# Performance work log

Hardware: AMD Instinct MI355X
Metric: run time of the kernel (lower is better)

## Reference

```python
import jax, jax.numpy as jnp
import numpy as np

N_NODES = 50000
N_EDGES = 800000
NFEAT, NHID, NCLASS = 512, 256, 128
N_UV = 2048


def gcn_layer(x, adj_row, adj_col, adj_val, W, b):
    # support = x @ W ; out = A @ support (sparse COO spmm) + b
    support = x @ W                                   # [N, out]
    msgs = adj_val[:, None] * support[adj_col]        # [E, out]
    out = jax.ops.segment_sum(msgs, adj_row, num_segments=N_NODES)
    return out + b


def setup_inputs() -> dict:
    key = jax.random.key(0)
    ks = jax.random.split(key, 12)
    u = jax.random.randint(ks[0], (N_UV,), 0, N_NODES)
    v = jax.random.randint(ks[1], (N_UV,), 0, N_NODES)
    x = jax.random.normal(ks[2], (N_NODES, NFEAT), dtype=jnp.float32)
    adj_row = jnp.sort(jax.random.randint(ks[3], (N_EDGES,), 0, N_NODES))
    adj_col = jax.random.randint(ks[4], (N_EDGES,), 0, N_NODES)
    adj_val = jax.random.uniform(ks[5], (N_EDGES,), dtype=jnp.float32)
    s1 = 1.0 / np.sqrt(NHID)
    s2 = 1.0 / np.sqrt(NCLASS)
    W1 = jax.random.uniform(ks[6], (NFEAT, NHID), minval=-s1, maxval=s1, dtype=jnp.float32)
    b1 = jax.random.uniform(ks[7], (NHID,), minval=-s1, maxval=s1, dtype=jnp.float32)
    W2 = jax.random.uniform(ks[8], (NHID, NCLASS), minval=-s2, maxval=s2, dtype=jnp.float32)
    b2 = jax.random.uniform(ks[9], (NCLASS,), minval=-s2, maxval=s2, dtype=jnp.float32)
    We = jax.random.normal(ks[10], (NCLASS, NCLASS), dtype=jnp.float32) * (1.0 / np.sqrt(NCLASS))
    return {"u": u, "v": v, "x": x, "adj_row": adj_row, "adj_col": adj_col,
            "adj_val": adj_val, "W1": W1, "b1": b1, "W2": W2, "b2": b2, "We": We}


def reference(u, v, x, adj_row, adj_col, adj_val, W1, b1, W2, b2, We):
    # layer 1: GCN + ReLU (dropout is identity in eval mode)
    h = jax.nn.relu(gcn_layer(x, adj_row, adj_col, adj_val, W1, b1))
    # layer 2: GCN
    z = gcn_layer(h, adj_row, adj_col, adj_val, W2, b2)          # [N, nclass]
    # edge scoring: sigmoid(w_edge(z[u]) @ z[v].T)
    zu = z[u] @ We.T                                             # [U, nclass] (nn.Linear: x @ W.T)
    zv = z[v]                                                    # [V, nclass]
    p_uv = jax.nn.sigmoid(zu @ zv.T)                             # [U, V]
    return p_uv
```

## Files before the change

### kernel.cpp

```cpp
#include <hip/hip_runtime.h>
#include <hip/hip_bf16.h>
#include <math.h>

#define N_NODES 50000
#define N_EDGES 800000
#define NFEAT   512
#define NHID    256
#define NCLASS  128
#define N_UV    2048

#define Q24_SCALE  524288.0f
#define Q24_INV    1.9073486328125e-6f

typedef __bf16    bf16x8 __attribute__((ext_vector_type(8)));
typedef short     s16x8  __attribute__((ext_vector_type(8)));
typedef float     f32x4  __attribute__((ext_vector_type(4)));

__device__ __forceinline__ unsigned short bf16_rn(float f) {
  unsigned u = __float_as_uint(f);
  u += 0x7fffu + ((u >> 16) & 1u);
  return (unsigned short)(u >> 16);
}
__device__ __forceinline__ float bf16_to_f(unsigned short h) {
  return __uint_as_float(((unsigned)h) << 16);
}

#define LDSPAD 40

template <bool ASPLIT, bool BSPLIT, int OMODE>
__global__ __launch_bounds__(256, 2) void gemm_mfma_split(
    const float* __restrict__ Af,
    const unsigned short* __restrict__ Ahi, const unsigned short* __restrict__ Alo,
    const float* __restrict__ BTf,
    const unsigned short* __restrict__ BThi, const unsigned short* __restrict__ BTlo,
    float* __restrict__ C, unsigned char* __restrict__ Cq, int M, int N, int K) {
  __shared__ unsigned short sAh[128 * LDSPAD];
  __shared__ unsigned short sAl[128 * LDSPAD];
  __shared__ unsigned short sBh[128 * LDSPAD];
  __shared__ unsigned short sBl[128 * LDSPAD];

  const int tid  = threadIdx.x;
  const int lane = tid & 63;
  const int wave = tid >> 6;
  const int wm   = (wave >> 1) << 6;
  const int wn   = (wave & 1) << 6;
  const int lm   = lane & 15;
  const int quad = lane >> 4;
  const int m0   = blockIdx.y * 128;
  const int n0   = blockIdx.x * 128;

  const int r32 = tid >> 3;
  const int c32 = (tid & 7) * 4;
  const int r16 = tid >> 2;
  const int c16 = (tid & 3) * 8;

  float4 pA[4]; s16x8 pAh[2], pAl[2];
  float4 pB[4]; s16x8 pBh[2], pBl[2];

  f32x4 acc[4][4];
#pragma unroll
  for (int i = 0; i < 4; ++i)
#pragma unroll
    for (int j = 0; j < 4; ++j)
#pragma unroll
      for (int r = 0; r < 4; ++r) acc[i][j][r] = 0.f;

#define LOAD_TILE(k0)                                                          \
  do {                                                                         \
    if (ASPLIT) {                                                              \
      _Pragma("unroll") for (int p = 0; p < 4; ++p) {                          \
        const int m = m0 + p * 32 + r32;                                       \
        pA[p] = make_float4(0.f, 0.f, 0.f, 0.f);                               \
        if (m < M) pA[p] = *(const float4*)&Af[(size_t)m * K + (k0) + c32];    \
      }                                                                        \
    } else {                                                                   \
      _Pragma("unroll") for (int p = 0; p < 2; ++p) {                          \
        const int m = m0 + p * 64 + r16;                                       \
        _Pragma("unroll") for (int e = 0; e < 8; ++e) { pAh[p][e] = 0; pAl[p][e] = 0; } \
        if (m < M) {                                                           \
          pAh[p] = *(const s16x8*)&Ahi[(size_t)m * K + (k0) + c16];            \
          pAl[p] = *(const s16x8*)&Alo[(size_t)m * K + (k0) + c16];            \
        }                                                                      \
      }                                                                        \
    }                                                                          \
    if (BSPLIT) {                                                              \
      _Pragma("unroll") for (int p = 0; p < 4; ++p) {                          \
        const int n = n0 + p * 32 + r32;                                       \
        pB[p] = *(const float4*)&BTf[(size_t)n * K + (k0) + c32];              \
      }                                                                        \
    } else {                                                                   \
      _Pragma("unroll") for (int p = 0; p < 2; ++p) {                          \
        pBh[p] = *(const s16x8*)&BThi[(size_t)(n0 + p * 64 + r16) * K + (k0) + c16]; \
        pBl[p] = *(const s16x8*)&BTlo[(size_t)(n0 + p * 64 + r16) * K + (k0) + c16]; \
      }                                                                        \
    }                                                                          \
  } while (0)

#define SPLIT4(v, hv, lv)                                                      \
  hv.x = bf16_rn(v.x); lv.x = bf16_rn(v.x - bf16_to_f(hv.x));                  \
  hv.y = bf16_rn(v.y); lv.y = bf16_rn(v.y - bf16_to_f(hv.y));                  \
  hv.z = bf16_rn(v.z); lv.z = bf16_rn(v.z - bf16_to_f(hv.z));                  \
  hv.w = bf16_rn(v.w); lv.w = bf16_rn(v.w - bf16_to_f(hv.w));

#define STORE_TILE()                                                           \
  do {                                                                         \
    if (ASPLIT) {                                                              \
      _Pragma("unroll") for (int p = 0; p < 4; ++p) {                          \
        ushort4 hv, lv; SPLIT4(pA[p], hv, lv);                                 \
        const int row = p * 32 + r32;                                          \
        *(ushort4*)&sAh[row * LDSPAD + c32] = hv;                              \
        *(ushort4*)&sAl[row * LDSPAD + c32] = lv;                              \
      }                                                                        \
    } else {                                                                   \
      _Pragma("unroll") for (int p = 0; p < 2; ++p) {                          \
        const int row = p * 64 + r16;                                          \
        *(s16x8*)&sAh[row * LDSPAD + c16] = pAh[p];                            \
        *(s16x8*)&sAl[row * LDSPAD + c16] = pAl[p];                            \
      }                                                                        \
    }                                                                          \
    if (BSPLIT) {                                                              \
      _Pragma("unroll") for (int p = 0; p < 4; ++p) {                          \
        ushort4 hv, lv; SPLIT4(pB[p], hv, lv);                                 \
        const int row = p * 32 + r32;                                          \
        *(ushort4*)&sBh[row * LDSPAD + c32] = hv;                              \
        *(ushort4*)&sBl[row * LDSPAD + c32] = lv;                              \
      }                                                                        \
    } else {                                                                   \
      _Pragma("unroll") for (int p = 0; p < 2; ++p) {                          \
        const int row = p * 64 + r16;                                          \
        *(s16x8*)&sBh[row * LDSPAD + c16] = pBh[p];                            \
        *(s16x8*)&sBl[row * LDSPAD + c16] = pBl[p];                            \
      }                                                                        \
    }                                                                          \
  } while (0)

  LOAD_TILE(0);

  for (int k0 = 0; k0 < K; k0 += 32) {
    if (k0) __syncthreads();
    STORE_TILE();
    __syncthreads();
    if (k0 + 32 < K) LOAD_TILE(k0 + 32);

    bf16x8 aH[4], aL[4], bH[4], bL[4];
#pragma unroll
    for (int i = 0; i < 4; ++i) {
      const int r = wm + i * 16 + lm;
      aH[i] = __builtin_bit_cast(bf16x8, *(const s16x8*)&sAh[r * LDSPAD + quad * 8]);
      aL[i] = __builtin_bit_cast(bf16x8, *(const s16x8*)&sAl[r * LDSPAD + quad * 8]);
    }
#pragma unroll
    for (int j = 0; j < 4; ++j) {
      const int r = wn + j * 16 + lm;
      bH[j] = __builtin_bit_cast(bf16x8, *(const s16x8*)&sBh[r * LDSPAD + quad * 8]);
      bL[j] = __builtin_bit_cast(bf16x8, *(const s16x8*)&sBl[r * LDSPAD + quad * 8]);
    }
#pragma unroll
    for (int i = 0; i < 4; ++i)
#pragma unroll
      for (int j = 0; j < 4; ++j) {
        acc[i][j] = __builtin_amdgcn_mfma_f32_16x16x32_bf16(aH[i], bH[j], acc[i][j], 0, 0, 0);
        acc[i][j] = __builtin_amdgcn_mfma_f32_16x16x32_bf16(aH[i], bL[j], acc[i][j], 0, 0, 0);
        acc[i][j] = __builtin_amdgcn_mfma_f32_16x16x32_bf16(aL[i], bH[j], acc[i][j], 0, 0, 0);
      }
  }

  const size_t qstride = (size_t)M * N;
#pragma unroll
  for (int i = 0; i < 4; ++i)
#pragma unroll
    for (int j = 0; j < 4; ++j) {
      const int col = n0 + wn + j * 16 + lm;
#pragma unroll
      for (int r = 0; r < 4; ++r) {
        const int row = m0 + wm + i * 16 + quad * 4 + r;
        if (row < M) {
          float v = acc[i][j][r];
          if (OMODE == 1) {
            v = 1.f / (1.f + expf(-v));
            C[(size_t)row * N + col] = v;
          } else if (OMODE == 2) {
            int q = __float2int_rn(v * Q24_SCALE);
            q = q > 8388607 ? 8388607 : (q < -8388608 ? -8388608 : q);
            const size_t o = (size_t)row * N + col;
            Cq[o]               = (unsigned char)(q & 0xFF);
            Cq[qstride + o]     = (unsigned char)((q >> 8) & 0xFF);
            Cq[2 * qstride + o] = (unsigned char)((q >> 16) & 0xFF);
          } else {
            C[(size_t)row * N + col] = v;
          }
        }
      }
    }
#undef LOAD_TILE
#undef STORE_TILE
#undef SPLIT4
}

__global__ __launch_bounds__(256) void prep_all(
    const int* __restrict__ rows, int* __restrict__ row_ptr,
    const float* __restrict__ W1, unsigned short* __restrict__ W1Thi,
    unsigned short* __restrict__ W1Tlo,
    const float* __restrict__ W2, unsigned short* __restrict__ W2Thi,
    unsigned short* __restrict__ W2Tlo) {
  const int idx = blockIdx.x * 256 + threadIdx.x;
  if (idx < N_EDGES) {
    const int r = rows[idx];
    const int rprev = (idx == 0) ? -1 : rows[idx - 1];
    for (int n = rprev + 1; n <= r; ++n) row_ptr[n] = idx;
    if (idx == N_EDGES - 1)
      for (int n = r + 1; n <= N_NODES; ++n) row_ptr[n] = N_EDGES;
  }
  if (idx < NFEAT * NHID) {
    const int n = idx / NFEAT;
    const int k = idx - n * NFEAT;
    const float f = W1[(size_t)k * NHID + n];
    const unsigned short h = bf16_rn(f);
    W1Thi[idx] = h;
    W1Tlo[idx] = bf16_rn(f - bf16_to_f(h));
  }
  if (idx < NHID * NCLASS) {
    const int n = idx / NHID;
    const int k = idx - n * NHID;
    const float f = W2[(size_t)k * NCLASS + n];
    const unsigned short h = bf16_rn(f);
    W2Thi[idx] = h;
    W2Tlo[idx] = bf16_rn(f - bf16_to_f(h));
  }
}

__global__ __launch_bounds__(256) void spmm256_q24p_split(
    const unsigned char* __restrict__ Sq, const int* __restrict__ row_ptr,
    const int* __restrict__ cols, const float* __restrict__ vals,
    const float4* __restrict__ bias4,
    unsigned short* __restrict__ outHi, unsigned short* __restrict__ outLo) {
  const size_t MN = (size_t)N_NODES * NHID;
  const int wave = threadIdx.x >> 6;
  const int lane = threadIdx.x & 63;
  const int node = blockIdx.x * 4 + wave;

  const int lo = row_ptr[node];
  const int hi = row_ptr[node + 1];

  float acc[4] = {0.f, 0.f, 0.f, 0.f};

#define ACCP(d0, d1, d2, ww)                                                   \
  do {                                                                         \
    const float ws = (ww) * Q24_INV;                                           \
    _Pragma("unroll") for (int i = 0; i < 4; ++i) {                            \
      const int q = ((int)((((d2) >> (8 * i)) & 0xFFu) << 24 |                 \
                           (((d1) >> (8 * i)) & 0xFFu) << 16 |                 \
                           (((d0) >> (8 * i)) & 0xFFu) << 8)) >> 8;            \
      acc[i] = fmaf(ws, (float)q, acc[i]);                                     \
    }                                                                          \
  } while (0)

  int e = lo;
  for (; e + 8 <= hi; e += 8) {
    int c[8]; float w[8];
#pragma unroll
    for (int t = 0; t < 8; ++t) { c[t] = cols[e + t]; w[t] = vals[e + t]; }
    unsigned d0[8], d1[8], d2[8];
#pragma unroll
    for (int t = 0; t < 8; ++t) {
      const size_t off = (size_t)c[t] * NHID + lane * 4;
      d0[t] = *(const unsigned*)&Sq[off];
      d1[t] = *(const unsigned*)&Sq[MN + off];
      d2[t] = *(const unsigned*)&Sq[2 * MN + off];
    }
#pragma unroll
    for (int t = 0; t < 8; ++t) ACCP(d0[t], d1[t], d2[t], w[t]);
  }
  for (; e < hi; ++e) {
    const size_t off = (size_t)cols[e] * NHID + lane * 4;
    const unsigned d0 = *(const unsigned*)&Sq[off];
    const unsigned d1 = *(const unsigned*)&Sq[MN + off];
    const unsigned d2 = *(const unsigned*)&Sq[2 * MN + off];
    ACCP(d0, d1, d2, vals[e]);
  }
#undef ACCP

  const float4 b = bias4[lane];
  float4 av;
  av.x = fmaxf(acc[0] + b.x, 0.f);
  av.y = fmaxf(acc[1] + b.y, 0.f);
  av.z = fmaxf(acc[2] + b.z, 0.f);
  av.w = fmaxf(acc[3] + b.w, 0.f);

  ushort4 hv, lv;
  hv.x = bf16_rn(av.x); lv.x = bf16_rn(av.x - bf16_to_f(hv.x));
  hv.y = bf16_rn(av.y); lv.y = bf16_rn(av.y - bf16_to_f(hv.y));
  hv.z = bf16_rn(av.z); lv.z = bf16_rn(av.z - bf16_to_f(hv.z));
  hv.w = bf16_rn(av.w); lv.w = bf16_rn(av.w - bf16_to_f(hv.w));
  const size_t o = (size_t)node * NHID + lane * 4;
  *(ushort4*)&outHi[o] = hv;
  *(ushort4*)&outLo[o] = lv;
}

__global__ __launch_bounds__(256) void spmm128_f32_list(
    const float4* __restrict__ S4, const int* __restrict__ row_ptr,
    const int* __restrict__ cols, const float* __restrict__ vals,
    const float4* __restrict__ bias4,
    const int* __restrict__ u, const int* __restrict__ v,
    float4* __restrict__ out4) {
  const int wave = threadIdx.x >> 6;
  const int lane = threadIdx.x & 63;
  const int half = lane >> 5;
  const int l32  = lane & 31;
  const int idx  = blockIdx.x * 4 + wave;
  const int node = idx < N_UV ? u[idx] : v[idx - N_UV];

  const int lo = row_ptr[node];
  const int hi = row_ptr[node + 1];

  float4 acc = make_float4(0.f, 0.f, 0.f, 0.f);
  int e = lo + half;
  for (; e + 6 < hi; e += 8) {
    int c[4]; float w[4];
#pragma unroll
    for (int t = 0; t < 4; ++t) { c[t] = cols[e + 2 * t]; w[t] = vals[e + 2 * t]; }
    float4 r[4];
#pragma unroll
    for (int t = 0; t < 4; ++t) r[t] = S4[(size_t)c[t] * 32 + l32];
#pragma unroll
    for (int t = 0; t < 4; ++t) {
      acc.x = fmaf(w[t], r[t].x, acc.x); acc.y = fmaf(w[t], r[t].y, acc.y);
      acc.z = fmaf(w[t], r[t].z, acc.z); acc.w = fmaf(w[t], r[t].w, acc.w);
    }
  }
  for (; e < hi; e += 2) {
    const int c = cols[e];
    const float w = vals[e];
    const float4 r = S4[(size_t)c * 32 + l32];
    acc.x = fmaf(w, r.x, acc.x); acc.y = fmaf(w, r.y, acc.y);
    acc.z = fmaf(w, r.z, acc.z); acc.w = fmaf(w, r.w, acc.w);
  }

  acc.x += __shfl_xor(acc.x, 32);
  acc.y += __shfl_xor(acc.y, 32);
  acc.z += __shfl_xor(acc.z, 32);
  acc.w += __shfl_xor(acc.w, 32);

  if (half == 0) {
    const float4 b = bias4[l32];
    acc.x += b.x; acc.y += b.y; acc.z += b.z; acc.w += b.w;
    out4[(size_t)idx * 32 + l32] = acc;
  }
}

extern "C" void kernel_launch(void* const* d_in, const int* in_sizes, int n_in,
                              void* d_out, int out_size, void* d_ws, size_t ws_size,
                              hipStream_t stream) {
  const int*   u       = (const int*)  d_in[0];
  const int*   v       = (const int*)  d_in[1];
  const float* x       = (const float*)d_in[2];
  const int*   adj_row = (const int*)  d_in[3];
  const int*   adj_col = (const int*)  d_in[4];
  const float* adj_val = (const float*)d_in[5];
  const float* W1      = (const float*)d_in[6];
  const float* b1      = (const float*)d_in[7];
  const float* W2      = (const float*)d_in[8];
  const float* b2      = (const float*)d_in[9];
  const float* We      = (const float*)d_in[10];
  float* out = (float*)d_out;

  char* wsb = (char*)d_ws;
  unsigned char* S1q = (unsigned char*)wsb;
  float* S2  = (float*)wsb;
  float* ZUV = (float*)(wsb + (size_t)N_NODES * NCLASS * sizeof(float));
  char* rB = wsb + (size_t)N_NODES * NHID * sizeof(float);
  unsigned short* Hhi = (unsigned short*)rB;
  unsigned short* Hlo = Hhi + (size_t)N_NODES * NHID;
  float* ZU = (float*)rB;
  unsigned short* W1Thi = (unsigned short*)out;
  unsigned short* W1Tlo = W1Thi + NHID * NFEAT;
  unsigned short* W2Thi = W1Tlo + NHID * NFEAT;
  unsigned short* W2Tlo = W2Thi + NCLASS * NHID;
  int* row_ptr = (int*)(W2Tlo + NCLASS * NHID);

  prep_all<<<(N_EDGES + 255) / 256, 256, 0, stream>>>(
      adj_row, row_ptr, W1, W1Thi, W1Tlo, W2, W2Thi, W2Tlo);

  gemm_mfma_split<true, false, 2>
      <<<dim3(NHID / 128, (N_NODES + 127) / 128), 256, 0, stream>>>(
      x, nullptr, nullptr, nullptr, W1Thi, W1Tlo,
      nullptr, S1q, N_NODES, NHID, NFEAT);

  spmm256_q24p_split<<<N_NODES / 4, 256, 0, stream>>>(
      S1q, row_ptr, adj_col, adj_val, (const float4*)b1, Hhi, Hlo);

  gemm_mfma_split<false, false, 0>
      <<<dim3(NCLASS / 128, (N_NODES + 127) / 128), 256, 0, stream>>>(
      nullptr, Hhi, Hlo, nullptr, W2Thi, W2Tlo,
      S2, nullptr, N_NODES, NCLASS, NHID);

  spmm128_f32_list<<<(2 * N_UV) / 4, 256, 0, stream>>>(
      (const float4*)S2, row_ptr, adj_col, adj_val, (const float4*)b2,
      u, v, (float4*)ZUV);

  gemm_mfma_split<true, true, 0>
      <<<dim3(NCLASS / 128, N_UV / 128), 256, 0, stream>>>(
      ZUV, nullptr, nullptr, We, nullptr, nullptr,
      ZU, nullptr, N_UV, NCLASS, NCLASS);

  gemm_mfma_split<true, true, 1>
      <<<dim3(N_UV / 128, N_UV / 128), 256, 0, stream>>>(
      ZU, nullptr, nullptr, ZUV + (size_t)N_UV * NCLASS, nullptr, nullptr,
      out, nullptr, N_UV, N_UV, NCLASS);
}
```

Baseline: 359.6 us.

## Interleave 24-bit support bytes per element and double GEMM K-tile to 64

The quantized 24-bit support matrix changes from three separate byte planes to a packed 3-byte-per-element layout, so each SpMM gather reads one 12-byte contiguous chunk instead of three 4-byte loads from distant planes. The GEMM K-step grows from 32 to 64, with padded LDS rows and two MFMA sub-steps per barrier, halving the number of sync/store rounds. The costs are byte-granular scattered stores in the GEMM epilogue, unaligned 12-byte loads, and roughly double the LDS and prefetch register use, which may cut occupancy.

```diff
diff --git a/kernel.cpp b/kernel.cpp
--- a/kernel.cpp
+++ b/kernel.cpp
@@ -16,6 +16,8 @@
 typedef short     s16x8  __attribute__((ext_vector_type(8)));
 typedef float     f32x4  __attribute__((ext_vector_type(4)));
 
+struct __attribute__((packed)) U3 { unsigned a, b, c; };
+
 __device__ __forceinline__ unsigned short bf16_rn(float f) {
   unsigned u = __float_as_uint(f);
   u += 0x7fffu + ((u >> 16) & 1u);
@@ -24,8 +26,15 @@
 __device__ __forceinline__ float bf16_to_f(unsigned short h) {
   return __uint_as_float(((unsigned)h) << 16);
 }
-
-#define LDSPAD 40
+__device__ __forceinline__ void unpack24(unsigned a, unsigned b, unsigned c,
+                                         int& e0, int& e1, int& e2, int& e3) {
+  e0 = ((int)(a << 8)) >> 8;
+  e1 = ((int)((b << 16) | ((a >> 24) << 8))) >> 8;
+  e2 = ((int)((c << 24) | ((b >> 16) << 8))) >> 8;
+  e3 = ((int)c) >> 8;
+}
+
+#define LDSPAD 72
 
 template <bool ASPLIT, bool BSPLIT, int OMODE>
 __global__ __launch_bounds__(256, 2) void gemm_mfma_split(
@@ -49,13 +58,13 @@
   const int m0   = blockIdx.y * 128;
   const int n0   = blockIdx.x * 128;
 
-  const int r32 = tid >> 3;
-  const int c32 = (tid & 7) * 4;
-  const int r16 = tid >> 2;
-  const int c16 = (tid & 3) * 8;
-
-  float4 pA[4]; s16x8 pAh[2], pAl[2];
-  float4 pB[4]; s16x8 pBh[2], pBl[2];
+  const int r32 = tid >> 4;
+  const int c32 = (tid & 15) * 4;
+  const int r16 = tid >> 3;
+  const int c16 = (tid & 7) * 8;
+
+  float4 pA[8]; s16x8 pAh[4], pAl[4];
+  float4 pB[8]; s16x8 pBh[4], pBl[4];
 
   f32x4 acc[4][4];
 #pragma unroll
@@ -68,14 +77,14 @@
 #define LOAD_TILE(k0)                                                          \
   do {                                                                         \
     if (ASPLIT) {                                                              \
-      _Pragma("unroll") for (int p = 0; p < 4; ++p) {                          \
-        const int m = m0 + p * 32 + r32;                                       \
+      _Pragma("unroll") for (int p = 0; p < 8; ++p) {                          \
+        const int m = m0 + p * 16 + r32;                                       \
         pA[p] = make_float4(0.f, 0.f, 0.f, 0.f);                               \
         if (m < M) pA[p] = *(const float4*)&Af[(size_t)m * K + (k0) + c32];    \
       }                                                                        \
     } else {                                                                   \
-      _Pragma("unroll") for (int p = 0; p < 2; ++p) {                          \
-        const int m = m0 + p * 64 + r16;                                       \
+      _Pragma("unroll") for (int p = 0; p < 4; ++p) {                          \
+        const int m = m0 + p * 32 + r16;                                       \
         _Pragma("unroll") for (int e = 0; e < 8; ++e) { pAh[p][e] = 0; pAl[p][e] = 0; } \
         if (m < M) {                                                           \
           pAh[p] = *(const s16x8*)&Ahi[(size_t)m * K + (k0) + c16];            \
@@ -84,14 +93,14 @@
       }                                                                        \
     }                                                                          \
     if (BSPLIT) {                                                              \
+      _Pragma("unroll") for (int p = 0; p < 8; ++p) {                          \
+        const int n = n0 + p * 16 + r32;                                       \
+        pB[p] = *(const float4*)&BTf[(size_t)n * K + (k0) + c32];              \
+      }                                                                        \
+    } else {                                                                   \
       _Pragma("unroll") for (int p = 0; p < 4; ++p) {                          \
-        const int n = n0 + p * 32 + r32;                                       \
-        pB[p] = *(const float4*)&BTf[(size_t)n * K + (k0) + c32];              \
-      }                                                                        \
-    } else {                                                                   \
-      _Pragma("unroll") for (int p = 0; p < 2; ++p) {                          \
-        pBh[p] = *(const s16x8*)&BThi[(size_t)(n0 + p * 64 + r16) * K + (k0) + c16]; \
-        pBl[p] = *(const s16x8*)&BTlo[(size_t)(n0 + p * 64 + r16) * K + (k0) + c16]; \
+        pBh[p] = *(const s16x8*)&BThi[(size_t)(n0 + p * 32 + r16) * K + (k0) + c16]; \
+        pBl[p] = *(const s16x8*)&BTlo[(size_t)(n0 + p * 32 + r16) * K + (k0) + c16]; \
       }                                                                        \
     }                                                                          \
   } while (0)
@@ -105,29 +114,29 @@
 #define STORE_TILE()                                                           \
   do {                                                                         \
     if (ASPLIT) {                                                              \
-      _Pragma("unroll") for (int p = 0; p < 4; ++p) {                          \
+      _Pragma("unroll") for (int p = 0; p < 8; ++p) {                          \
         ushort4 hv, lv; SPLIT4(pA[p], hv, lv);                                 \
-        const int row = p * 32 + r32;                                          \
+        const int row = p * 16 + r32;                                          \
         *(ushort4*)&sAh[row * LDSPAD + c32] = hv;                              \
         *(ushort4*)&sAl[row * LDSPAD + c32] = lv;                              \
       }                                                                        \
     } else {                                                                   \
-      _Pragma("unroll") for (int p = 0; p < 2; ++p) {                          \
-        const int row = p * 64 + r16;                                          \
+      _Pragma("unroll") for (int p = 0; p < 4; ++p) {                          \
+        const int row = p * 32 + r16;                                          \
         *(s16x8*)&sAh[row * LDSPAD + c16] = pAh[p];                            \
         *(s16x8*)&sAl[row * LDSPAD + c16] = pAl[p];                            \
       }                                                                        \
     }                                                                          \
     if (BSPLIT) {                                                              \
-      _Pragma("unroll") for (int p = 0; p < 4; ++p) {                          \
+      _Pragma("unroll") for (int p = 0; p < 8; ++p) {                          \
         ushort4 hv, lv; SPLIT4(pB[p], hv, lv);                                 \
-        const int row = p * 32 + r32;                                          \
+        const int row = p * 16 + r32;                                          \
         *(ushort4*)&sBh[row * LDSPAD + c32] = hv;                              \
         *(ushort4*)&sBl[row * LDSPAD + c32] = lv;                              \
       }                                                                        \
     } else {                                                                   \
-      _Pragma("unroll") for (int p = 0; p < 2; ++p) {                          \
-        const int row = p * 64 + r16;                                          \
+      _Pragma("unroll") for (int p = 0; p < 4; ++p) {                          \
+        const int row = p * 32 + r16;                                          \
         *(s16x8*)&sBh[row * LDSPAD + c16] = pBh[p];                            \
         *(s16x8*)&sBl[row * LDSPAD + c16] = pBl[p];                            \
       }                                                                        \
@@ -136,36 +145,39 @@
 
   LOAD_TILE(0);
 
-  for (int k0 = 0; k0 < K; k0 += 32) {
+  for (int k0 = 0; k0 < K; k0 += 64) {
     if (k0) __syncthreads();
     STORE_TILE();
     __syncthreads();
-    if (k0 + 32 < K) LOAD_TILE(k0 + 32);
-
-    bf16x8 aH[4], aL[4], bH[4], bL[4];
-#pragma unroll
-    for (int i = 0; i < 4; ++i) {
-      const int r = wm + i * 16 + lm;
-      aH[i] = __builtin_bit_cast(bf16x8, *(const s16x8*)&sAh[r * LDSPAD + quad * 8]);
-      aL[i] = __builtin_bit_cast(bf16x8, *(const s16x8*)&sAl[r * LDSPAD + quad * 8]);
+    if (k0 + 64 < K) LOAD_TILE(k0 + 64);
+
+#pragma unroll
+    for (int ks = 0; ks < 2; ++ks) {
+      const int koff = ks * 32 + quad * 8;
+      bf16x8 aH[4], aL[4], bH[4], bL[4];
+#pragma unroll
+      for (int i = 0; i < 4; ++i) {
+        const int r = wm + i * 16 + lm;
+        aH[i] = __builtin_bit_cast(bf16x8, *(const s16x8*)&sAh[r * LDSPAD + koff]);
+        aL[i] = __builtin_bit_cast(bf16x8, *(const s16x8*)&sAl[r * LDSPAD + koff]);
+      }
+#pragma unroll
+      for (int j = 0; j < 4; ++j) {
+        const int r = wn + j * 16 + lm;
+        bH[j] = __builtin_bit_cast(bf16x8, *(const s16x8*)&sBh[r * LDSPAD + koff]);
+        bL[j] = __builtin_bit_cast(bf16x8, *(const s16x8*)&sBl[r * LDSPAD + koff]);
+      }
+#pragma unroll
+      for (int i = 0; i < 4; ++i)
+#pragma unroll
+        for (int j = 0; j < 4; ++j) {
+          acc[i][j] = __builtin_amdgcn_mfma_f32_16x16x32_bf16(aH[i], bH[j], acc[i][j], 0, 0, 0);
+          acc[i][j] = __builtin_amdgcn_mfma_f32_16x16x32_bf16(aH[i], bL[j], acc[i][j], 0, 0, 0);
+          acc[i][j] = __builtin_amdgcn_mfma_f32_16x16x32_bf16(aL[i], bH[j], acc[i][j], 0, 0, 0);
+        }
     }
-#pragma unroll
-    for (int j = 0; j < 4; ++j) {
-      const int r = wn + j * 16 + lm;
-      bH[j] = __builtin_bit_cast(bf16x8, *(const s16x8*)&sBh[r * LDSPAD + quad * 8]);
-      bL[j] = __builtin_bit_cast(bf16x8, *(const s16x8*)&sBl[r * LDSPAD + quad * 8]);
-    }
-#pragma unroll
-    for (int i = 0; i < 4; ++i)
-#pragma unroll
-      for (int j = 0; j < 4; ++j) {
-        acc[i][j] = __builtin_amdgcn_mfma_f32_16x16x32_bf16(aH[i], bH[j], acc[i][j], 0, 0, 0);
-        acc[i][j] = __builtin_amdgcn_mfma_f32_16x16x32_bf16(aH[i], bL[j], acc[i][j], 0, 0, 0);
-        acc[i][j] = __builtin_amdgcn_mfma_f32_16x16x32_bf16(aL[i], bH[j], acc[i][j], 0, 0, 0);
-      }
-  }
-
-  const size_t qstride = (size_t)M * N;
+  }
+
 #pragma unroll
   for (int i = 0; i < 4; ++i)
 #pragma unroll
@@ -182,10 +194,10 @@
           } else if (OMODE == 2) {
             int q = __float2int_rn(v * Q24_SCALE);
             q = q > 8388607 ? 8388607 : (q < -8388608 ? -8388608 : q);
-            const size_t o = (size_t)row * N + col;
-            Cq[o]               = (unsigned char)(q & 0xFF);
-            Cq[qstride + o]     = (unsigned char)((q >> 8) & 0xFF);
-            Cq[2 * qstride + o] = (unsigned char)((q >> 16) & 0xFF);
+            unsigned char* p = Cq + ((size_t)row * N + col) * 3;
+            p[0] = (unsigned char)(q & 0xFF);
+            p[1] = (unsigned char)((q >> 8) & 0xFF);
+            p[2] = (unsigned char)((q >> 16) & 0xFF);
           } else {
             C[(size_t)row * N + col] = v;
           }
@@ -229,12 +241,11 @@
   }
 }
 
-__global__ __launch_bounds__(256) void spmm256_q24p_split(
+__global__ __launch_bounds__(256) void spmm256_q24_split(
     const unsigned char* __restrict__ Sq, const int* __restrict__ row_ptr,
     const int* __restrict__ cols, const float* __restrict__ vals,
     const float4* __restrict__ bias4,
     unsigned short* __restrict__ outHi, unsigned short* __restrict__ outLo) {
-  const size_t MN = (size_t)N_NODES * NHID;
   const int wave = threadIdx.x >> 6;
   const int lane = threadIdx.x & 63;
   const int node = blockIdx.x * 4 + wave;
@@ -242,17 +253,17 @@
   const int lo = row_ptr[node];
   const int hi = row_ptr[node + 1];
 
-  float acc[4] = {0.f, 0.f, 0.f, 0.f};
-
-#define ACCP(d0, d1, d2, ww)                                                   \
+  float4 acc = make_float4(0.f, 0.f, 0.f, 0.f);
+
+#define ACCQ(dd, ww)                                                           \
   do {                                                                         \
+    int e0, e1, e2, e3;                                                        \
+    unpack24((dd).a, (dd).b, (dd).c, e0, e1, e2, e3);                          \
     const float ws = (ww) * Q24_INV;                                           \
-    _Pragma("unroll") for (int i = 0; i < 4; ++i) {                            \
-      const int q = ((int)((((d2) >> (8 * i)) & 0xFFu) << 24 |                 \
-                           (((d1) >> (8 * i)) & 0xFFu) << 16 |                 \
-                           (((d0) >> (8 * i)) & 0xFFu) << 8)) >> 8;            \
-      acc[i] = fmaf(ws, (float)q, acc[i]);                                     \
-    }                                                                          \
+    acc.x = fmaf(ws, (float)e0, acc.x);                                        \
+    acc.y = fmaf(ws, (float)e1, acc.y);                                        \
+    acc.z = fmaf(ws, (float)e2, acc.z);                                        \
+    acc.w = fmaf(ws, (float)e3, acc.w);                                        \
   } while (0)
 
   int e = lo;
@@ -260,38 +271,30 @@
     int c[8]; float w[8];
 #pragma unroll
     for (int t = 0; t < 8; ++t) { c[t] = cols[e + t]; w[t] = vals[e + t]; }
-    unsigned d0[8], d1[8], d2[8];
-#pragma unroll
-    for (int t = 0; t < 8; ++t) {
-      const size_t off = (size_t)c[t] * NHID + lane * 4;
-      d0[t] = *(const unsigned*)&Sq[off];
-      d1[t] = *(const unsigned*)&Sq[MN + off];
-      d2[t] = *(const unsigned*)&Sq[2 * MN + off];
-    }
-#pragma unroll
-    for (int t = 0; t < 8; ++t) ACCP(d0[t], d1[t], d2[t], w[t]);
+    U3 d[8];
+#pragma unroll
+    for (int t = 0; t < 8; ++t)
+      d[t] = *(const U3*)&Sq[(size_t)c[t] * (NHID * 3) + lane * 12];
+#pragma unroll
+    for (int t = 0; t < 8; ++t) ACCQ(d[t], w[t]);
   }
   for (; e < hi; ++e) {
-    const size_t off = (size_t)cols[e] * NHID + lane * 4;
-    const unsigned d0 = *(const unsigned*)&Sq[off];
-    const unsigned d1 = *(const unsigned*)&Sq[MN + off];
-    const unsigned d2 = *(const unsigned*)&Sq[2 * MN + off];
-    ACCP(d0, d1, d2, vals[e]);
-  }
-#undef ACCP
+    const U3 d = *(const U3*)&Sq[(size_t)cols[e] * (NHID * 3) + lane * 12];
+    ACCQ(d, vals[e]);
+  }
+#undef ACCQ
 
   const float4 b = bias4[lane];
-  float4 av;
-  av.x = fmaxf(acc[0] + b.x, 0.f);
-  av.y = fmaxf(acc[1] + b.y, 0.f);
-  av.z = fmaxf(acc[2] + b.z, 0.f);
-  av.w = fmaxf(acc[3] + b.w, 0.f);
+  acc.x = fmaxf(acc.x + b.x, 0.f);
+  acc.y = fmaxf(acc.y + b.y, 0.f);
+  acc.z = fmaxf(acc.z + b.z, 0.f);
+  acc.w = fmaxf(acc.w + b.w, 0.f);
 
   ushort4 hv, lv;
-  hv.x = bf16_rn(av.x); lv.x = bf16_rn(av.x - bf16_to_f(hv.x));
-  hv.y = bf16_rn(av.y); lv.y = bf16_rn(av.y - bf16_to_f(hv.y));
-  hv.z = bf16_rn(av.z); lv.z = bf16_rn(av.z - bf16_to_f(hv.z));
-  hv.w = bf16_rn(av.w); lv.w = bf16_rn(av.w - bf16_to_f(hv.w));
+  hv.x = bf16_rn(acc.x); lv.x = bf16_rn(acc.x - bf16_to_f(hv.x));
+  hv.y = bf16_rn(acc.y); lv.y = bf16_rn(acc.y - bf16_to_f(hv.y));
+  hv.z = bf16_rn(acc.z); lv.z = bf16_rn(acc.z - bf16_to_f(hv.z));
+  hv.w = bf16_rn(acc.w); lv.w = bf16_rn(acc.w - bf16_to_f(hv.w));
   const size_t o = (size_t)node * NHID + lane * 4;
   *(ushort4*)&outHi[o] = hv;
   *(ushort4*)&outLo[o] = lv;
@@ -386,7 +389,7 @@
       x, nullptr, nullptr, nullptr, W1Thi, W1Tlo,
       nullptr, S1q, N_NODES, NHID, NFEAT);
 
-  spmm256_q24p_split<<<N_NODES / 4, 256, 0, stream>>>(
+  spmm256_q24_split<<<N_NODES / 4, 256, 0, stream>>>(
       S1q, row_ptr, adj_col, adj_val, (const float4*)b1, Hhi, Hlo);
 
   gemm_mfma_split<false, false, 0>
```

Result: no change. 355.4 us (-1.2%).
